# Performance work log

Hardware: AMD Instinct MI355X
Metric: run time of the kernel (lower is better)

## Reference

```python
import jax, jax.numpy as jnp
import numpy as np
from jax.scipy.linalg import expm

N = 8
FS = 48000
NFFT = FS * 8              # irfft length, hardcoded in the module
F = NFFT // 2 + 1          # one-sided spectrum length = 192001
GAIN_PER_SAMPLE = 0.9999
_DELAYS = np.array([809., 877., 937., 1049., 1151., 1249., 1373., 1499.], dtype=np.float32)
M_AVR = float(_DELAYS.mean())
M_STD = float(_DELAYS.std(ddof=1))  # torch.std is unbiased


def setup_inputs() -> dict:
    key = jax.random.key(0)
    kB, kC, kW = jax.random.split(key, 3)
    # frequency grid on the upper unit circle, z = e^{i w}, w in [0, pi]
    w = jnp.linspace(0.0, np.pi, F).astype(jnp.float32)
    x = jnp.exp(1j * w).astype(jnp.complex64)
    B = (jax.random.normal(kB, (N, 1), dtype=jnp.float32) / N)
    C = (jax.random.normal(kC, (N,), dtype=jnp.float32) / N)
    W = jax.random.normal(kW, (N, N), dtype=jnp.float32)  # seed for Skew+MatrixExponential parametrization
    m = jnp.asarray((_DELAYS - M_AVR) / M_STD)            # normalized delays (learnable)
    return {"x": x, "B": B, "C": C, "W": W, "m": m}


def reference(x, B, C, W, m):
    # A = expm(skew(W)), an orthogonal feedback matrix  [N,N]
    S = jnp.triu(W, 1)
    A = expm(S - S.T)
    # de-normalize delays
    md = m * M_STD + M_AVR                                # [N]
    gamma = jnp.power(GAIN_PER_SAMPLE, md)                # [N] real
    # D(z) = diag(z^m)  per frequency  -> [F,N] complex
    xm = jnp.power(x[:, None], md[None, :].astype(jnp.complex64))
    # M = D - A @ Gamma ; A @ diag(gamma) == A * gamma (column scaling)
    AG = (A * gamma[None, :]).astype(jnp.complex64)       # [N,N]
    eye = jnp.eye(N, dtype=jnp.complex64)
    Mmat = xm[:, None, :] * eye - AG[None, :, :]          # [F,N,N]
    # Hchannel = inv(M) @ B  (solved, same math as inverse+matmul)
    Bc = jnp.broadcast_to(B.astype(jnp.complex64), (F, N, 1))
    Hch = jnp.linalg.solve(Mmat, Bc)[:, :, 0]             # [F,N]
    H = Hch * C[None, :].astype(jnp.complex64)            # [F,N]
    Hsum = jnp.sum(H, axis=-1)                            # [F]
    mask = jnp.where(x == 0, 0.0, 1.0).astype(Hsum.real.dtype)
    h = jnp.fft.irfft(Hsum * mask, n=NFFT)                # [NFFT] real
    h = h / jnp.max(jnp.abs(h))
    return H, h
```

## Files before the change

kernel.cpp:

```cpp
#include <hip/hip_runtime.h>
#include <math.h>

#define F_LEN 192001
#define NFFT  384000
#define MHALF 192000
#define NCH   8

__device__ __forceinline__ float2 cmulf(float2 a, float2 b) {
  return make_float2(a.x*b.x - a.y*b.y, a.x*b.y + a.y*b.x);
}
__device__ __forceinline__ float2 caddf2(float2 a, float2 b){ return make_float2(a.x+b.x, a.y+b.y); }
__device__ __forceinline__ float2 csubf2(float2 a, float2 b){ return make_float2(a.x-b.x, a.y-b.y); }

__global__ __launch_bounds__(64) void precompute_kernel(
    const float* __restrict__ W, const float* __restrict__ m,
    double* __restrict__ md_d, float* __restrict__ AG, unsigned int* __restrict__ mxbits)
{
  __shared__ double S[64], P[64], T[64];
  __shared__ double norm_sh;
  const int t = threadIdx.x;
  const int i = t >> 3, j = t & 7;

  double wij = (j > i) ? (double)W[i*8+j] : 0.0;
  double wji = (i > j) ? (double)W[j*8+i] : 0.0;
  S[t] = wij - wji;
  __syncthreads();

  if (t == 0) {
    double best = 0.0;
    for (int r = 0; r < 8; ++r) {
      double rs = 0.0;
      for (int c = 0; c < 8; ++c) rs += fabs(S[r*8+c]);
      best = fmax(best, rs);
    }
    norm_sh = best;
  }
  __syncthreads();

  double nrm = norm_sh;
  int s = 0;
  while (nrm > 0.5 && s < 60) { nrm *= 0.5; ++s; }
  S[t] *= ldexp(1.0, -s);

  P[t] = (i == j) ? 1.0 : 0.0;
  T[t] = P[t];
  __syncthreads();

  for (int k = 1; k <= 13; ++k) {
    double acc = 0.0;
    #pragma unroll
    for (int l = 0; l < 8; ++l) acc += T[i*8+l] * S[l*8+j];
    __syncthreads();
    T[t] = acc / (double)k;
    P[t] += T[t];
    __syncthreads();
  }
  for (int q = 0; q < s; ++q) {
    double acc = 0.0;
    #pragma unroll
    for (int l = 0; l < 8; ++l) acc += P[i*8+l] * P[l*8+j];
    __syncthreads();
    P[t] = acc;
    __syncthreads();
  }

  const double M_AVR = 1118.0;
  const double M_STDd = (double)((float)sqrt(419520.0 / 7.0));
  const double LN_GAIN = log(0.9999);

  double md_j  = (double)m[j] * M_STDd + M_AVR;
  double gam_j = exp(md_j * LN_GAIN);
  AG[t] = (float)(P[t] * gam_j);

  if (t < 8) md_d[t] = (double)m[t] * M_STDd + M_AVR;
  if (t == 0) *mxbits = 0u;
}

__global__ __launch_bounds__(256) void freq_solve_kernel(
    const double* __restrict__ md_d, const float* __restrict__ AG,
    const float* __restrict__ Bp, const float* __restrict__ Cp,
    float* __restrict__ outH, float2* __restrict__ Y, int interleaved)
{
  int f = blockIdx.x * blockDim.x + threadIdx.x;
  if (f >= F_LEN) return;

  const double TWO_PI = 6.283185307179586476925287;
  double fd = (double)f;
  float xc[8], xs[8];
  #pragma unroll
  for (int n = 0; n < 8; ++n) {
    double tt = fd * md_d[n] * (1.0 / (double)NFFT);
    tt -= floor(tt);
    float ang = (float)(tt * TWO_PI);
    __sincosf(ang, &xs[n], &xc[n]);
  }

  float2 Mm[8][8];
  float2 yv[8];
  float2 idg[8];
  #pragma unroll
  for (int i = 0; i < 8; ++i) {
    #pragma unroll
    for (int j = 0; j < 8; ++j) {
      float2 v = make_float2(-AG[i*8+j], 0.0f);
      if (i == j) { v.x += xc[i]; v.y = xs[i]; }
      Mm[i][j] = v;
    }
    yv[i] = make_float2(Bp[i], 0.0f);
  }

  #pragma unroll
  for (int k = 0; k < 8; ++k) {
    float2 p = Mm[k][k];
    float rd = 1.0f / (p.x*p.x + p.y*p.y);
    float2 inv = make_float2(p.x*rd, -p.y*rd);
    idg[k] = inv;
    #pragma unroll
    for (int i = k+1; i < 8; ++i) {
      float2 fm = cmulf(Mm[i][k], inv);
      #pragma unroll
      for (int j = k+1; j < 8; ++j)
        Mm[i][j] = csubf2(Mm[i][j], cmulf(fm, Mm[k][j]));
      yv[i] = csubf2(yv[i], cmulf(fm, yv[k]));
    }
  }
  #pragma unroll
  for (int k = 7; k >= 0; --k) {
    float2 acc = yv[k];
    #pragma unroll
    for (int j = k+1; j < 8; ++j)
      acc = csubf2(acc, cmulf(Mm[k][j], yv[j]));
    yv[k] = cmulf(acc, idg[k]);
  }

  float2 hsum = make_float2(0.f, 0.f);
  #pragma unroll
  for (int n = 0; n < 8; ++n) {
    float c = Cp[n];
    float2 H = make_float2(yv[n].x * c, yv[n].y * c);
    yv[n] = H;
    hsum = caddf2(hsum, H);
  }

  if (interleaved) {
    float2* o = (float2*)outH;
    #pragma unroll
    for (int n = 0; n < 8; ++n) o[f*8+n] = yv[n];
  } else {
    #pragma unroll
    for (int n = 0; n < 8; ++n) outH[f*8+n] = yv[n].x;
  }

  Y[f] = hsum;
}

__device__ __forceinline__ void dft4_inv(float2* v) {
  float2 t0 = caddf2(v[0], v[2]);
  float2 t1 = csubf2(v[0], v[2]);
  float2 t2 = caddf2(v[1], v[3]);
  float2 t3 = csubf2(v[1], v[3]);
  float2 it3 = make_float2(-t3.y, t3.x);
  v[0] = caddf2(t0, t2);
  v[1] = caddf2(t1, it3);
  v[2] = csubf2(t0, t2);
  v[3] = csubf2(t1, it3);
}

__device__ __forceinline__ void dft3_inv(float2* v) {
  const float S3 = 0.86602540378443864676f;
  float2 t1 = caddf2(v[1], v[2]);
  float2 d  = csubf2(v[1], v[2]);
  float2 u  = make_float2(v[0].x - 0.5f*t1.x, v[0].y - 0.5f*t1.y);
  float2 idd = make_float2(-S3*d.y, S3*d.x);
  v[0] = caddf2(v[0], t1);
  v[1] = caddf2(u, idd);
  v[2] = csubf2(u, idd);
}

__device__ __forceinline__ void dft5_inv(float2* v) {
  const float C1 =  0.30901699437494742410f;
  const float S1 =  0.95105651629515357212f;
  const float C2 = -0.80901699437494742410f;
  const float S2 =  0.58778525229247312917f;
  float2 t1 = caddf2(v[1], v[4]);
  float2 t2 = caddf2(v[2], v[3]);
  float2 t3 = csubf2(v[1], v[4]);
  float2 t4 = csubf2(v[2], v[3]);
  float2 x0 = v[0];
  float2 a1 = make_float2(x0.x + C1*t1.x + C2*t2.x, x0.y + C1*t1.y + C2*t2.y);
  float2 b1 = make_float2(S1*t3.x + S2*t4.x,        S1*t3.y + S2*t4.y);
  float2 a2 = make_float2(x0.x + C2*t1.x + C1*t2.x, x0.y + C2*t1.y + C1*t2.y);
  float2 b2 = make_float2(S2*t3.x - S1*t4.x,        S2*t3.y - S1*t4.y);
  float2 ib1 = make_float2(-b1.y, b1.x);
  float2 ib2 = make_float2(-b2.y, b2.x);
  v[0] = make_float2(x0.x + t1.x + t2.x, x0.y + t1.y + t2.y);
  v[1] = caddf2(a1, ib1);
  v[4] = csubf2(a1, ib1);
  v[2] = caddf2(a2, ib2);
  v[3] = csubf2(a2, ib2);
}

__device__ __forceinline__ void dft8_inv(float2* v) {
  const float HF = 0.70710678118654752440f;
  float2 e[4] = {v[0], v[2], v[4], v[6]};
  float2 o[4] = {v[1], v[3], v[5], v[7]};
  dft4_inv(e); dft4_inv(o);
  o[1] = cmulf(o[1], make_float2(HF, HF));
  o[2] = make_float2(-o[2].y, o[2].x);
  o[3] = cmulf(o[3], make_float2(-HF, HF));
  #pragma unroll
  for (int k = 0; k < 4; ++k) {
    v[k]   = caddf2(e[k], o[k]);
    v[k+4] = csubf2(e[k], o[k]);
  }
}

__device__ __forceinline__ void dft15_inv(float2* v) {
  float2 a[5][3];
  #pragma unroll
  for (int n2 = 0; n2 < 5; ++n2) {
    #pragma unroll
    for (int n1 = 0; n1 < 3; ++n1)
      a[n2][n1] = v[(5*n1 + 3*n2) % 15];
    dft3_inv(a[n2]);
  }
  #pragma unroll
  for (int k1 = 0; k1 < 3; ++k1) {
    float2 b[5];
    #pragma unroll
    for (int n2 = 0; n2 < 5; ++n2) b[n2] = a[n2][k1];
    dft5_inv(b);
    #pragma unroll
    for (int k2 = 0; k2 < 5; ++k2) v[(10*k1 + 6*k2) % 15] = b[k2];
  }
}

__device__ __constant__ float TW25[25][2] = {
  { 1.0f, 0.0f },
  { 0.9685831611286311f,  0.2486898871648548f },
  { 0.8763066800438636f,  0.4817536741017153f },
  { 0.7289686274214116f,  0.6845471059286887f },
  { 0.5358267949789967f,  0.8443279255020151f },
  { 0.3090169943749474f,  0.9510565162951535f },
  { 0.0627905195293134f,  0.9980267284282716f },
  {-0.1873813145857246f,  0.9822872507286887f },
  {-0.4257792915650727f,  0.9048270524660196f },
  {-0.6374239897486896f,  0.7705132427757893f },
  {-0.8090169943749474f,  0.5877852522924731f },
  {-0.9297764858882515f,  0.3681245526846780f },
  {-0.9921147013144779f,  0.1253332335643043f },
  {-0.9921147013144779f, -0.1253332335643043f },
  {-0.9297764858882515f, -0.3681245526846780f },
  {-0.8090169943749474f, -0.5877852522924731f },
  {-0.6374239897486899f, -0.7705132427757891f },
  {-0.4257792915650727f, -0.9048270524660196f },
  {-0.1873813145857246f, -0.9822872507286887f },
  { 0.0627905195293134f, -0.9980267284282716f },
  { 0.3090169943749474f, -0.9510565162951535f },
  { 0.5358267949789967f, -0.8443279255020151f },
  { 0.7289686274214116f, -0.6845471059286887f },
  { 0.8763066800438636f, -0.4817536741017153f },
  { 0.9685831611286311f, -0.2486898871648548f },
};

__device__ __forceinline__ void dft25_inv(float2* v) {
  float2 a[5][5];
  #pragma unroll
  for (int n2 = 0; n2 < 5; ++n2) {
    float2 b[5];
    #pragma unroll
    for (int n1 = 0; n1 < 5; ++n1) b[n1] = v[5*n1 + n2];
    dft5_inv(b);
    #pragma unroll
    for (int k1 = 0; k1 < 5; ++k1) a[k1][n2] = b[k1];
  }
  #pragma unroll
  for (int k1 = 1; k1 < 5; ++k1) {
    #pragma unroll
    for (int n2 = 1; n2 < 5; ++n2) {
      const int mm = (n2 * k1) % 25;
      a[k1][n2] = cmulf(a[k1][n2], make_float2(TW25[mm][0], TW25[mm][1]));
    }
  }
  #pragma unroll
  for (int k1 = 0; k1 < 5; ++k1) {
    dft5_inv(a[k1]);
    #pragma unroll
    for (int k2 = 0; k2 < 5; ++k2) v[k1 + 5*k2] = a[k1][k2];
  }
}

__global__ __launch_bounds__(192) void fftA_kernel(
    const float2* __restrict__ Y, float2* __restrict__ out)
{
  __shared__ float2 lds[3][576];
  const int wave = threadIdx.x >> 6;
  const int l = threadIdx.x & 63;
  const int d = blockIdx.x * 3 + wave;
  float2* A = lds[wave];
  const double TWO_PI = 6.283185307179586476925287;

  float2 v[8];
  #pragma unroll
  for (int r = 0; r < 8; ++r) {
    int t = l + 64*r;
    int n = d + 375*t;
    float2 Ya = Y[n];
    float2 Ym = Y[MHALF - n];
    if (n == 0) { Ya.y = 0.f; Ym.y = 0.f; }
    float2 E  = make_float2(Ya.x + Ym.x, Ya.y - Ym.y);
    float2 Oc = make_float2(Ya.x - Ym.x, Ya.y + Ym.y);
    double tt = (double)n * (1.0 / (double)NFFT);
    float ang = (float)(TWO_PI * tt);
    float sn, cs; __sincosf(ang, &sn, &cs);
    float2 O = make_float2(cs*Oc.x - sn*Oc.y, cs*Oc.y + sn*Oc.x);
    v[r] = make_float2(E.x - O.y, E.y + O.x);
  }
  dft8_inv(v);
  #pragma unroll
  for (int r = 0; r < 8; ++r) { int idx = 8*l + r; A[idx + (idx>>3)] = v[r]; }
  __syncthreads();

  {
    int jm = l & 7, jd = l >> 3;
    #pragma unroll
    for (int r = 0; r < 8; ++r) { int idx = l + 64*r; v[r] = A[idx + (idx>>3)]; }
    double tb = (double)jm * (1.0/64.0);
    #pragma unroll
    for (int r = 1; r < 8; ++r) {
      float ang = (float)(TWO_PI * tb * (double)r);
      float sn, cs; __sincosf(ang, &sn, &cs);
      v[r] = cmulf(v[r], make_float2(cs, sn));
    }
    dft8_inv(v);
    __syncthreads();
    #pragma unroll
    for (int r = 0; r < 8; ++r) { int idx = jd*64 + jm + 8*r; A[idx + (idx>>3)] = v[r]; }
  }
  __syncthreads();

  {
    #pragma unroll
    for (int r = 0; r < 8; ++r) { int idx = l + 64*r; v[r] = A[idx + (idx>>3)]; }
    double tb = (double)l * (1.0/512.0);
    #pragma unroll
    for (int r = 1; r < 8; ++r) {
      float ang = (float)(TWO_PI * tb * (double)r);
      float sn, cs; __sincosf(ang, &sn, &cs);
      v[r] = cmulf(v[r], make_float2(cs, sn));
    }
    dft8_inv(v);
    #pragma unroll
    for (int r = 0; r < 8; ++r) out[d*512 + l + 64*r] = v[r];
  }
}

__global__ __launch_bounds__(256) void fftB_kernel(
    const float2* __restrict__ Ain, float2* __restrict__ out, unsigned int* __restrict__ mx)
{
  __shared__ float2 lds[375*9];
  const int tid = threadIdx.x;
  const int J0 = blockIdx.x * 8;
  const double TWO_PI = 6.283185307179586476925287;

  #pragma unroll
  for (int k = 0; k < 12; ++k) {
    int i = tid + 256*k;
    if (i < 3000) {
      int d = i >> 3, jl = i & 7;
      lds[d*9 + jl] = Ain[d*512 + J0 + jl];
    }
  }
  __syncthreads();

  {
    bool act = tid < 200;
    int jl = tid & 7, jd = tid >> 3;
    float2 p[15];
    if (act) {
      #pragma unroll
      for (int r = 0; r < 15; ++r) p[r] = lds[(jd + 25*r)*9 + jl];
    }
    __syncthreads();
    if (act) {
      int jm = J0 + jl;
      double tb = (double)jm * (1.0/7680.0);
      #pragma unroll
      for (int r = 1; r < 15; ++r) {
        float ang = (float)(TWO_PI * tb * (double)r);
        float sn, cs; __sincosf(ang, &sn, &cs);
        p[r] = cmulf(p[r], make_float2(cs, sn));
      }
      dft15_inv(p);
      #pragma unroll
      for (int r = 0; r < 15; ++r) lds[(15*jd + r)*9 + jl] = p[r];
    }
  }
  __syncthreads();

  float mloc = 0.f;
  {
    bool act = tid < 120;
    int jl = tid & 7, s = tid >> 3;
    float2 q[25];
    if (act) {
      #pragma unroll
      for (int r = 0; r < 25; ++r) q[r] = lds[(s + 15*r)*9 + jl];
      int jm = J0 + jl;
      int j = jm + 512*s;
      double tb = (double)j * (1.0/(double)MHALF);
      #pragma unroll
      for (int r = 1; r < 25; ++r) {
        float ang = (float)(TWO_PI * tb * (double)r);
        float sn, cs; __sincosf(ang, &sn, &cs);
        q[r] = cmulf(q[r], make_float2(cs, sn));
      }
      dft25_inv(q);
      #pragma unroll
      for (int r = 0; r < 25; ++r) {
        out[jm + 512*(s + 15*r)] = q[r];
        mloc = fmaxf(mloc, fmaxf(fabsf(q[r].x), fabsf(q[r].y)));
      }
    }
  }
  #pragma unroll
  for (int off = 32; off > 0; off >>= 1)
    mloc = fmaxf(mloc, __shfl_xor(mloc, off));
  if ((tid & 63) == 0) atomicMax(mx, __float_as_uint(mloc));
}

__global__ __launch_bounds__(256) void norm_kernel(
    const float4* __restrict__ z, const unsigned int* __restrict__ mx,
    float4* __restrict__ hout)
{
  int n = blockIdx.x * blockDim.x + threadIdx.x;
  if (n >= MHALF/2) return;
  float r = 1.0f / __uint_as_float(*mx);
  float4 zz = z[n];
  hout[n] = make_float4(zz.x*r, zz.y*r, zz.z*r, zz.w*r);
}

extern "C" void kernel_launch(void* const* d_in, const int* in_sizes, int n_in,
                              void* d_out, int out_size, void* d_ws, size_t ws_size,
                              hipStream_t stream)
{
  const float* Bp = (const float*)d_in[1];
  const float* Cp = (const float*)d_in[2];
  const float* Wp = (const float*)d_in[3];
  const float* mp = (const float*)d_in[4];

  char* ws = (char*)d_ws;
  double* md_d = (double*)ws;
  float*  AG   = (float*)(ws + 64);
  unsigned int* mx = (unsigned int*)(ws + 384);
  float2* bufY = (float2*)(ws + 512);
  float2* bufA = (float2*)(ws + 512 + 1536128);
  float2* bufB = bufA + MHALF;

  float* outf = (float*)d_out;
  const int hoff = out_size - NFFT;
  const int interleaved = (hoff >= 2 * F_LEN * NCH) ? 1 : 0;

  precompute_kernel<<<1, 64, 0, stream>>>(Wp, mp, md_d, AG, mx);
  freq_solve_kernel<<<(F_LEN + 255) / 256, 256, 0, stream>>>(
      md_d, AG, Bp, Cp, outf, bufY, interleaved);

  fftA_kernel<<<125, 192, 0, stream>>>(bufY, bufA);
  fftB_kernel<<<64, 256, 0, stream>>>(bufA, bufB, mx);

  norm_kernel<<<(MHALF/2 + 255)/256, 256, 0, stream>>>(
      (const float4*)bufB, mx, (float4*)(outf + hoff));
}
```

Before: 37.58 us.

## Fuse normalization into final FFT stage via grid-wide spin barrier

The separate norm kernel is removed. The last FFT stage now keeps its results in registers, publishes a block max, and waits on a global atomic counter until all 64 blocks have arrived. It then reads the global max and writes the scaled output directly. This saves one launch plus a full round trip of the intermediate buffer through memory. The per-frequency H output stores are also widened from float2 to float4. The spin barrier only works if all 64 blocks are resident at the same time, which 64 blocks on this GPU should allow.

```diff
diff --git a/kernel.cpp b/kernel.cpp
--- a/kernel.cpp
+++ b/kernel.cpp
@@ -14,7 +14,8 @@
 
 __global__ __launch_bounds__(64) void precompute_kernel(
     const float* __restrict__ W, const float* __restrict__ m,
-    double* __restrict__ md_d, float* __restrict__ AG, unsigned int* __restrict__ mxbits)
+    double* __restrict__ md_d, float* __restrict__ AG,
+    unsigned int* __restrict__ mxbits, unsigned int* __restrict__ done)
 {
   __shared__ double S[64], P[64], T[64];
   __shared__ double norm_sh;
@@ -73,7 +74,7 @@
   AG[t] = (float)(P[t] * gam_j);
 
   if (t < 8) md_d[t] = (double)m[t] * M_STDd + M_AVR;
-  if (t == 0) *mxbits = 0u;
+  if (t == 0) { *mxbits = 0u; *done = 0u; }
 }
 
 __global__ __launch_bounds__(256) void freq_solve_kernel(
@@ -143,9 +144,10 @@
   }
 
   if (interleaved) {
-    float2* o = (float2*)outH;
-    #pragma unroll
-    for (int n = 0; n < 8; ++n) o[f*8+n] = yv[n];
+    float4* o = (float4*)outH;
+    #pragma unroll
+    for (int n = 0; n < 4; ++n)
+      o[f*4+n] = make_float4(yv[2*n].x, yv[2*n].y, yv[2*n+1].x, yv[2*n+1].y);
   } else {
     #pragma unroll
     for (int n = 0; n < 8; ++n) outH[f*8+n] = yv[n].x;
@@ -356,7 +358,8 @@
 }
 
 __global__ __launch_bounds__(256) void fftB_kernel(
-    const float2* __restrict__ Ain, float2* __restrict__ out, unsigned int* __restrict__ mx)
+    const float2* __restrict__ Ain, float2* __restrict__ hout,
+    unsigned int* __restrict__ mx, unsigned int* __restrict__ done)
 {
   __shared__ float2 lds[375*9];
   const int tid = threadIdx.x;
@@ -398,46 +401,48 @@
   }
   __syncthreads();
 
+  const bool act = tid < 120;
+  const int jl = tid & 7, s = tid >> 3;
+  const int jm = J0 + jl;
+  float2 q[25];
   float mloc = 0.f;
-  {
-    bool act = tid < 120;
-    int jl = tid & 7, s = tid >> 3;
-    float2 q[25];
-    if (act) {
-      #pragma unroll
-      for (int r = 0; r < 25; ++r) q[r] = lds[(s + 15*r)*9 + jl];
-      int jm = J0 + jl;
-      int j = jm + 512*s;
-      double tb = (double)j * (1.0/(double)MHALF);
-      #pragma unroll
-      for (int r = 1; r < 25; ++r) {
-        float ang = (float)(TWO_PI * tb * (double)r);
-        float sn, cs; __sincosf(ang, &sn, &cs);
-        q[r] = cmulf(q[r], make_float2(cs, sn));
-      }
-      dft25_inv(q);
-      #pragma unroll
-      for (int r = 0; r < 25; ++r) {
-        out[jm + 512*(s + 15*r)] = q[r];
-        mloc = fmaxf(mloc, fmaxf(fabsf(q[r].x), fabsf(q[r].y)));
-      }
-    }
+  if (act) {
+    #pragma unroll
+    for (int r = 0; r < 25; ++r) q[r] = lds[(s + 15*r)*9 + jl];
+    int j = jm + 512*s;
+    double tb = (double)j * (1.0/(double)MHALF);
+    #pragma unroll
+    for (int r = 1; r < 25; ++r) {
+      float ang = (float)(TWO_PI * tb * (double)r);
+      float sn, cs; __sincosf(ang, &sn, &cs);
+      q[r] = cmulf(q[r], make_float2(cs, sn));
+    }
+    dft25_inv(q);
+    #pragma unroll
+    for (int r = 0; r < 25; ++r)
+      mloc = fmaxf(mloc, fmaxf(fabsf(q[r].x), fabsf(q[r].y)));
   }
   #pragma unroll
   for (int off = 32; off > 0; off >>= 1)
     mloc = fmaxf(mloc, __shfl_xor(mloc, off));
   if ((tid & 63) == 0) atomicMax(mx, __float_as_uint(mloc));
-}
-
-__global__ __launch_bounds__(256) void norm_kernel(
-    const float4* __restrict__ z, const unsigned int* __restrict__ mx,
-    float4* __restrict__ hout)
-{
-  int n = blockIdx.x * blockDim.x + threadIdx.x;
-  if (n >= MHALF/2) return;
-  float r = 1.0f / __uint_as_float(*mx);
-  float4 zz = z[n];
-  hout[n] = make_float4(zz.x*r, zz.y*r, zz.z*r, zz.w*r);
+
+  __syncthreads();
+  if (tid == 0) {
+    __threadfence();
+    atomicAdd(done, 1u);
+    while (__hip_atomic_load(done, __ATOMIC_ACQUIRE, __HIP_MEMORY_SCOPE_AGENT)
+           < gridDim.x) { __builtin_amdgcn_s_sleep(1); }
+  }
+  __syncthreads();
+
+  float rinv = 1.0f / __uint_as_float(
+      __hip_atomic_load(mx, __ATOMIC_ACQUIRE, __HIP_MEMORY_SCOPE_AGENT));
+  if (act) {
+    #pragma unroll
+    for (int r = 0; r < 25; ++r)
+      hout[jm + 512*(s + 15*r)] = make_float2(q[r].x * rinv, q[r].y * rinv);
+  }
 }
 
 extern "C" void kernel_launch(void* const* d_in, const int* in_sizes, int n_in,
@@ -452,22 +457,19 @@
   char* ws = (char*)d_ws;
   double* md_d = (double*)ws;
   float*  AG   = (float*)(ws + 64);
-  unsigned int* mx = (unsigned int*)(ws + 384);
+  unsigned int* mx   = (unsigned int*)(ws + 384);
+  unsigned int* done = (unsigned int*)(ws + 448);
   float2* bufY = (float2*)(ws + 512);
   float2* bufA = (float2*)(ws + 512 + 1536128);
-  float2* bufB = bufA + MHALF;
 
   float* outf = (float*)d_out;
   const int hoff = out_size - NFFT;
   const int interleaved = (hoff >= 2 * F_LEN * NCH) ? 1 : 0;
 
-  precompute_kernel<<<1, 64, 0, stream>>>(Wp, mp, md_d, AG, mx);
+  precompute_kernel<<<1, 64, 0, stream>>>(Wp, mp, md_d, AG, mx, done);
   freq_solve_kernel<<<(F_LEN + 255) / 256, 256, 0, stream>>>(
       md_d, AG, Bp, Cp, outf, bufY, interleaved);
 
   fftA_kernel<<<125, 192, 0, stream>>>(bufY, bufA);
-  fftB_kernel<<<64, 256, 0, stream>>>(bufA, bufB, mx);
-
-  norm_kernel<<<(MHALF/2 + 255)/256, 256, 0, stream>>>(
-      (const float4*)bufB, mx, (float4*)(outf + hoff));
-}
+  fftB_kernel<<<64, 256, 0, stream>>>(bufA, (float2*)(outf + hoff), mx, done);
+}
```

After: 41.11 us. 1.09x slower.

## Fuse matrix-exponential precompute into per-frequency solve kernel, use fast reciprocal

Applied to the files above, without the earlier changes.

The single-block precompute kernel (expm of the skew matrix, gamma scaling, delay de-normalization) is removed. Every block of the frequency solve kernel now recomputes these small values redundantly into shared memory, which saves one kernel launch and its serialization point. In exchange, each of about 750 blocks runs roughly 30 double-precision barrier-synchronized steps before starting its own work. The pivot reciprocal also switches to the hardware rcp instruction, which is less accurate than an IEEE divide.

```diff
diff --git a/kernel.cpp b/kernel.cpp
--- a/kernel.cpp
+++ b/kernel.cpp
@@ -12,76 +12,96 @@
 __device__ __forceinline__ float2 caddf2(float2 a, float2 b){ return make_float2(a.x+b.x, a.y+b.y); }
 __device__ __forceinline__ float2 csubf2(float2 a, float2 b){ return make_float2(a.x-b.x, a.y-b.y); }
 
-__global__ __launch_bounds__(64) void precompute_kernel(
+__device__ __forceinline__ float frcp_fast(float x) {
+#if __has_builtin(__builtin_amdgcn_rcpf)
+  return __builtin_amdgcn_rcpf(x);
+#else
+  return 1.0f / x;
+#endif
+}
+
+__global__ __launch_bounds__(256) void freq_solve_kernel(
     const float* __restrict__ W, const float* __restrict__ m,
-    double* __restrict__ md_d, float* __restrict__ AG, unsigned int* __restrict__ mxbits)
+    const float* __restrict__ Bp, const float* __restrict__ Cp,
+    float* __restrict__ outH, float2* __restrict__ Y,
+    unsigned int* __restrict__ mxbits, int interleaved)
 {
   __shared__ double S[64], P[64], T[64];
   __shared__ double norm_sh;
-  const int t = threadIdx.x;
-  const int i = t >> 3, j = t & 7;
-
-  double wij = (j > i) ? (double)W[i*8+j] : 0.0;
-  double wji = (i > j) ? (double)W[j*8+i] : 0.0;
-  S[t] = wij - wji;
-  __syncthreads();
-
-  if (t == 0) {
-    double best = 0.0;
-    for (int r = 0; r < 8; ++r) {
-      double rs = 0.0;
-      for (int c = 0; c < 8; ++c) rs += fabs(S[r*8+c]);
-      best = fmax(best, rs);
-    }
-    norm_sh = best;
-  }
-  __syncthreads();
-
-  double nrm = norm_sh;
-  int s = 0;
-  while (nrm > 0.5 && s < 60) { nrm *= 0.5; ++s; }
-  S[t] *= ldexp(1.0, -s);
-
-  P[t] = (i == j) ? 1.0 : 0.0;
-  T[t] = P[t];
-  __syncthreads();
-
-  for (int k = 1; k <= 13; ++k) {
-    double acc = 0.0;
-    #pragma unroll
-    for (int l = 0; l < 8; ++l) acc += T[i*8+l] * S[l*8+j];
-    __syncthreads();
-    T[t] = acc / (double)k;
-    P[t] += T[t];
-    __syncthreads();
-  }
-  for (int q = 0; q < s; ++q) {
-    double acc = 0.0;
-    #pragma unroll
-    for (int l = 0; l < 8; ++l) acc += P[i*8+l] * P[l*8+j];
-    __syncthreads();
-    P[t] = acc;
-    __syncthreads();
-  }
-
-  const double M_AVR = 1118.0;
-  const double M_STDd = (double)((float)sqrt(419520.0 / 7.0));
-  const double LN_GAIN = log(0.9999);
-
-  double md_j  = (double)m[j] * M_STDd + M_AVR;
-  double gam_j = exp(md_j * LN_GAIN);
-  AG[t] = (float)(P[t] * gam_j);
-
-  if (t < 8) md_d[t] = (double)m[t] * M_STDd + M_AVR;
-  if (t == 0) *mxbits = 0u;
-}
-
-__global__ __launch_bounds__(256) void freq_solve_kernel(
-    const double* __restrict__ md_d, const float* __restrict__ AG,
-    const float* __restrict__ Bp, const float* __restrict__ Cp,
-    float* __restrict__ outH, float2* __restrict__ Y, int interleaved)
-{
-  int f = blockIdx.x * blockDim.x + threadIdx.x;
+  __shared__ float AGs[64];
+  __shared__ double md_s[8];
+
+  const int tid = threadIdx.x;
+  if (blockIdx.x == 0 && tid == 0) *mxbits = 0u;
+
+  {
+    const bool t64 = tid < 64;
+    const int i = (tid >> 3) & 7, j = tid & 7;
+    if (t64) {
+      double wij = (j > i) ? (double)W[i*8+j] : 0.0;
+      double wji = (i > j) ? (double)W[j*8+i] : 0.0;
+      S[tid] = wij - wji;
+    }
+    __syncthreads();
+
+    if (tid == 0) {
+      double best = 0.0;
+      for (int r = 0; r < 8; ++r) {
+        double rs = 0.0;
+        for (int c = 0; c < 8; ++c) rs += fabs(S[r*8+c]);
+        best = fmax(best, rs);
+      }
+      norm_sh = best;
+    }
+    __syncthreads();
+
+    double nrm = norm_sh;
+    int s = 0;
+    while (nrm > 0.5 && s < 60) { nrm *= 0.5; ++s; }
+    if (t64) {
+      S[tid] *= ldexp(1.0, -s);
+      P[tid] = (i == j) ? 1.0 : 0.0;
+      T[tid] = P[tid];
+    }
+    __syncthreads();
+
+    for (int k = 1; k <= 13; ++k) {
+      double acc = 0.0;
+      if (t64) {
+        #pragma unroll
+        for (int l = 0; l < 8; ++l) acc += T[i*8+l] * S[l*8+j];
+      }
+      __syncthreads();
+      if (t64) {
+        T[tid] = acc / (double)k;
+        P[tid] += T[tid];
+      }
+      __syncthreads();
+    }
+    for (int q = 0; q < s; ++q) {
+      double acc = 0.0;
+      if (t64) {
+        #pragma unroll
+        for (int l = 0; l < 8; ++l) acc += P[i*8+l] * P[l*8+j];
+      }
+      __syncthreads();
+      if (t64) P[tid] = acc;
+      __syncthreads();
+    }
+
+    const double M_AVR = 1118.0;
+    const double M_STDd = (double)((float)sqrt(419520.0 / 7.0));
+    const double LN_GAIN = log(0.9999);
+    if (t64) {
+      double md_j  = (double)m[j] * M_STDd + M_AVR;
+      double gam_j = exp(md_j * LN_GAIN);
+      AGs[tid] = (float)(P[tid] * gam_j);
+      if (tid < 8) md_s[tid] = (double)m[tid] * M_STDd + M_AVR;
+    }
+    __syncthreads();
+  }
+
+  int f = blockIdx.x * blockDim.x + tid;
   if (f >= F_LEN) return;
 
   const double TWO_PI = 6.283185307179586476925287;
@@ -89,7 +109,7 @@
   float xc[8], xs[8];
   #pragma unroll
   for (int n = 0; n < 8; ++n) {
-    double tt = fd * md_d[n] * (1.0 / (double)NFFT);
+    double tt = fd * md_s[n] * (1.0 / (double)NFFT);
     tt -= floor(tt);
     float ang = (float)(tt * TWO_PI);
     __sincosf(ang, &xs[n], &xc[n]);
@@ -102,7 +122,7 @@
   for (int i = 0; i < 8; ++i) {
     #pragma unroll
     for (int j = 0; j < 8; ++j) {
-      float2 v = make_float2(-AG[i*8+j], 0.0f);
+      float2 v = make_float2(-AGs[i*8+j], 0.0f);
       if (i == j) { v.x += xc[i]; v.y = xs[i]; }
       Mm[i][j] = v;
     }
@@ -112,7 +132,7 @@
   #pragma unroll
   for (int k = 0; k < 8; ++k) {
     float2 p = Mm[k][k];
-    float rd = 1.0f / (p.x*p.x + p.y*p.y);
+    float rd = frcp_fast(p.x*p.x + p.y*p.y);
     float2 inv = make_float2(p.x*rd, -p.y*rd);
     idg[k] = inv;
     #pragma unroll
@@ -450,8 +470,6 @@
   const float* mp = (const float*)d_in[4];
 
   char* ws = (char*)d_ws;
-  double* md_d = (double*)ws;
-  float*  AG   = (float*)(ws + 64);
   unsigned int* mx = (unsigned int*)(ws + 384);
   float2* bufY = (float2*)(ws + 512);
   float2* bufA = (float2*)(ws + 512 + 1536128);
@@ -461,9 +479,8 @@
   const int hoff = out_size - NFFT;
   const int interleaved = (hoff >= 2 * F_LEN * NCH) ? 1 : 0;
 
-  precompute_kernel<<<1, 64, 0, stream>>>(Wp, mp, md_d, AG, mx);
   freq_solve_kernel<<<(F_LEN + 255) / 256, 256, 0, stream>>>(
-      md_d, AG, Bp, Cp, outf, bufY, interleaved);
+      Wp, mp, Bp, Cp, outf, bufY, mx, interleaved);
 
   fftA_kernel<<<125, 192, 0, stream>>>(bufY, bufA);
   fftB_kernel<<<64, 256, 0, stream>>>(bufA, bufB, mx);
```

Measured after the change: 39.18 us. 1.04x slower.
